# Performance work log

Hardware: AMD Instinct MI355X
Metric: run time of the kernel (lower is better)

The kernel has to match this reference:

```python
import jax, jax.numpy as jnp
import numpy as np

EPS = 1e-10


def setup_inputs() -> dict:
    key = jax.random.key(0)
    k1, k2 = jax.random.split(key)
    B, C, H, W = 8, 16, 256, 256
    x = jax.random.normal(k1, (B, C, H, W), dtype=jnp.float32)
    # grid_sample-style normalized coords in [-1, 1]
    inv_grid = jax.random.uniform(k2, (B, H, W, 2), dtype=jnp.float32, minval=-1.0, maxval=1.0)
    return {"x": x, "inv_grid": inv_grid}


def reference(x, inv_grid):
    B, C, Hin, Win = x.shape
    h, w = Hin, Win  # OH = OW = None -> output size equals input size

    g = (inv_grid + 1.0) * 0.5
    # coord 0 scaled by h, coord 1 by w, shifted by +1 (padding row/col), clamped
    ci = jnp.clip(g[..., 0] * h + 1.0, 0.0, h + 1 - 2 * EPS)
    cj = jnp.clip(g[..., 1] * w + 1.0, 0.0, w + 1 - 2 * EPS)
    i0 = jnp.floor(ci).astype(jnp.int32)  # coords >= 0 so floor == trunc (.long())
    j0 = jnp.floor(cj).astype(jnp.int32)

    # broadcast over channel dim (grid is shared across channels)
    ci_ = ci[:, None]
    cj_ = cj[:, None]
    i0_ = i0[:, None]
    j0_ = j0[:, None]

    bidx = jnp.arange(B)[:, None, None, None]
    cidx = jnp.arange(C)[None, :, None, None]

    A = jnp.zeros((B, C, h + 3, w + 3), dtype=x.dtype)
    for di in range(2):
        wi = jax.nn.relu(1.0 - jnp.abs(ci_ - (i0_ + di).astype(ci_.dtype)))
        for dj in range(2):
            wj = jax.nn.relu(1.0 - jnp.abs(cj_ - (j0_ + dj).astype(cj_.dtype)))
            # bilinear splat scatter-add of x * weight into the 4 corner cells
            A = A.at[bidx, cidx, i0_ + di, j0_ + dj].add(x * (wi * wj))
    return A[..., 1:h + 1, 1:w + 1]
```

## Files before the change

### kernel.cpp

```cpp
#include <hip/hip_runtime.h>
#include <hip/hip_fp16.h>
#include <stdint.h>

#define BB 8
#define CC 16
#define HH 256
#define WW 256
#define HW (HH * WW)
#define NSRC (BB * HW)
#define NBLK (NSRC / 256)
#define MAXSLOT 15
#define CNT_BYTES ((size_t)NSRC * 4)


__global__ __launch_bounds__(256) void pass1_bin(
    const float* __restrict__ inv_grid,
    uint32_t* __restrict__ counts,
    uint2* __restrict__ srcs)
{
    const int idx = blockIdx.x * 256 + threadIdx.x;
    const float2 g2 = ((const float2*)inv_grid)[idx];
    const float ci = fminf(fmaxf(fmaf((g2.x + 1.0f) * 0.5f, (float)HH, 1.0f), 0.0f), 257.0f);
    const float cj = fminf(fmaxf(fmaf((g2.y + 1.0f) * 0.5f, (float)WW, 1.0f), 0.0f), 257.0f);
    const int i0 = (int)floorf(ci);
    const int j0 = (int)floorf(cj);
    const float fi = ci - (float)i0;
    const float fj = cj - (float)j0;
    const int bi = i0 - 1, bj = j0 - 1;
    uint32_t meta = 0xFFFFFFFFu;
    if (((unsigned)bi < HH) & ((unsigned)bj < WW)) {
        const int b = idx >> 16;
        const uint32_t bin = (b << 16) | (bi << 8) | bj;
        const uint32_t slot = atomicAdd(&counts[bin], 1u);
        if (slot < MAXSLOT) meta = (bin << 4) | slot;
    }
    const uint32_t fi16 = (uint32_t)(fi * 65535.0f + 0.5f);
    const uint32_t fj16 = (uint32_t)(fj * 65535.0f + 0.5f);
    uint2 m; m.x = meta; m.y = fi16 | (fj16 << 16);
    srcs[idx] = m;
}

__global__ __launch_bounds__(256) void scanA(
    const uint32_t* __restrict__ counts,
    uint32_t* __restrict__ co,
    uint32_t* __restrict__ cursors)
{
    const int t    = threadIdx.x;
    const int lane = t & 63;
    const int wv   = t >> 6;
    const int blk  = blockIdx.x;
    const int i    = blk * 256 + t;
    const uint32_t v = counts[i];

    uint32_t s = v;
#pragma unroll
    for (int d = 1; d < 64; d <<= 1) {
        const uint32_t u = __shfl_up(s, (unsigned)d, 64);
        if (lane >= d) s += u;
    }

    __shared__ uint32_t wsum[4];
    __shared__ uint32_t gbase_s;
    if (lane == 63) wsum[wv] = s;
    __syncthreads();

    uint32_t base = 0;
#pragma unroll
    for (int w = 0; w < 3; ++w)
        if (w < wv) base += wsum[w];

    if (t == 255) {
        const int b = blk >> 8;
        gbase_s = ((uint32_t)b << 16) + atomicAdd(&cursors[b * 64], base + s);
    }
    __syncthreads();

    const uint32_t excl = base + s - v + gbase_s;
    co[i] = (excl << 4) | min(v, 15u);
}

__global__ __launch_bounds__(256) void fill_records(
    const float* __restrict__ x,
    const uint2* __restrict__ srcs,
    const uint32_t* __restrict__ co,
    uint32_t* __restrict__ ff,
    uint4* __restrict__ pl)
{
    const int idx = blockIdx.x * 256 + threadIdx.x;
    const uint2 m = srcs[idx];
    if (m.x == 0xFFFFFFFFu) return;
    const uint32_t bin  = m.x >> 4;
    const uint32_t slot = m.x & 15u;
    const uint32_t pos  = (co[bin] >> 4) + slot;

    const int b = idx >> 16;
    const int p = idx & 0xFFFF;
    const float* xp = x + (((size_t)b * CC) << 16) + p;

    uint32_t h[8];
#pragma unroll
    for (int q = 0; q < 8; ++q) {
        const float v0 = xp[(size_t)(2 * q)     << 16];
        const float v1 = xp[(size_t)(2 * q + 1) << 16];
        const uint32_t h0 = (uint32_t)__half_as_ushort(__float2half_rn(v0));
        const uint32_t h1 = (uint32_t)__half_as_ushort(__float2half_rn(v1));
        h[q] = h0 | (h1 << 16);
    }
    ff[pos] = m.y;
    uint4 q0; q0.x = h[0]; q0.y = h[1]; q0.z = h[2]; q0.w = h[3];
    uint4 q1; q1.x = h[4]; q1.y = h[5]; q1.z = h[6]; q1.w = h[7];
    pl[(size_t)pos * 2]     = q0;
    pl[(size_t)pos * 2 + 1] = q1;
}

__global__ __launch_bounds__(256) void gather_csr(
    const uint32_t* __restrict__ co,
    const uint32_t* __restrict__ ff,
    const uint4* __restrict__ pl,
    float* __restrict__ out)
{
    const int g   = blockIdx.x;
    const int b   = g & 7;
    const int seq = g >> 3;
    const int r   = ((seq >> 4) << 4) + (threadIdx.x >> 4);
    const int c   = ((seq & 15) << 4) + (threadIdx.x & 15);

    uint32_t hdr[4];
#pragma unroll
    for (int q = 0; q < 4; ++q) {
        const int row = r + (q >> 1) - 1;
        const int col = c + (q & 1) - 1;
        const bool val = (row >= 0) & (col >= 0);
        const uint32_t rr   = val ? (uint32_t)row : 0u;
        const uint32_t ccol = val ? (uint32_t)col : 0u;
        const uint32_t bin = ((uint32_t)b << 16) | (rr << 8) | ccol;
        const uint32_t m = co[bin];
        hdr[q] = val ? m : (m & ~15u);
    }

    float acc[CC];
#pragma unroll
    for (int q = 0; q < CC; ++q) acc[q] = 0.0f;

#pragma unroll
    for (int q = 0; q < 4; ++q) {
        const uint32_t cnt = hdr[q] & 15u;
        const uint32_t off = hdr[q] >> 4;
        for (uint32_t k = 0; k < cnt; ++k) {
            const size_t pos = (size_t)(off + k);
            const uint32_t f2 = ff[pos];
            const uint4 p0 = pl[pos * 2];
            const uint4 p1 = pl[pos * 2 + 1];
            const float fi = (float)(f2 & 0xFFFFu) * (1.0f / 65535.0f);
            const float fj = (float)(f2 >> 16)     * (1.0f / 65535.0f);
            const float wi = (q & 2) ? (1.0f - fi) : fi;
            const float wj = (q & 1) ? (1.0f - fj) : fj;
            const float w = wi * wj;
            const uint32_t hs[8] = {p0.x, p0.y, p0.z, p0.w, p1.x, p1.y, p1.z, p1.w};
#pragma unroll
            for (int qq = 0; qq < 8; ++qq) {
                const float v0 = __half2float(__ushort_as_half((unsigned short)(hs[qq] & 0xFFFFu)));
                const float v1 = __half2float(__ushort_as_half((unsigned short)(hs[qq] >> 16)));
                acc[2 * qq]     += w * v0;
                acc[2 * qq + 1] += w * v1;
            }
        }
    }

    float* op = out + (((size_t)(b * CC)) << 16) + (r << 8) + c;
#pragma unroll
    for (int q = 0; q < CC; ++q)
        op[(size_t)q << 16] = acc[q];
}

__global__ __launch_bounds__(256) void invgrid_scatter_direct(
    const float* __restrict__ x,
    const float* __restrict__ inv_grid,
    float* __restrict__ out)
{
    const int idx = blockIdx.x * 256 + threadIdx.x;
    const int b = idx >> 16;
    const float2 g2 = ((const float2*)inv_grid)[idx];
    const float ci = fminf(fmaxf(fmaf((g2.x + 1.0f) * 0.5f, (float)HH, 1.0f), 0.0f), 257.0f);
    const float cj = fminf(fmaxf(fmaf((g2.y + 1.0f) * 0.5f, (float)WW, 1.0f), 0.0f), 257.0f);
    const int i0 = (int)floorf(ci);
    const int j0 = (int)floorf(cj);
    const float wi0 = fmaxf(0.0f, 1.0f - fabsf(ci - (float)i0));
    const float wi1 = fmaxf(0.0f, 1.0f - fabsf(ci - (float)(i0 + 1)));
    const float wj0 = fmaxf(0.0f, 1.0f - fabsf(cj - (float)j0));
    const float wj1 = fmaxf(0.0f, 1.0f - fabsf(cj - (float)(j0 + 1)));
    const float w00 = wi0 * wj0, w01 = wi0 * wj1;
    const float w10 = wi1 * wj0, w11 = wi1 * wj1;
    const int r0 = i0 - 1, r1 = i0, c0 = j0 - 1, c1 = j0;
    const bool vr0 = (unsigned)r0 < HH, vr1 = (unsigned)r1 < HH;
    const bool vc0 = (unsigned)c0 < WW, vc1 = (unsigned)c1 < WW;
    const int o00 = r0 * WW + c0, o01 = r0 * WW + c1;
    const int o10 = r1 * WW + c0, o11 = r1 * WW + c1;
    const int p = idx & 0xFFFF;
    const float* xp = x + (size_t)b * CC * HW + p;
    float* op = out + (size_t)b * CC * HW;
#pragma unroll
    for (int cch = 0; cch < CC; ++cch) {
        const float xv = xp[(size_t)cch * HW];
        float* ob = op + (size_t)cch * HW;
        if (vr0 & vc0) atomicAdd(ob + o00, xv * w00);
        if (vr0 & vc1) atomicAdd(ob + o01, xv * w01);
        if (vr1 & vc0) atomicAdd(ob + o10, xv * w10);
        if (vr1 & vc1) atomicAdd(ob + o11, xv * w11);
    }
}

extern "C" void kernel_launch(void* const* d_in, const int* in_sizes, int n_in,
                              void* d_out, int out_size, void* d_ws, size_t ws_size,
                              hipStream_t stream) {
    const float* x        = (const float*)d_in[0];
    const float* inv_grid = (const float*)d_in[1];
    float* out            = (float*)d_out;

    const size_t A = 256;
    size_t o_counts  = 0;
    size_t o_cursors = CNT_BYTES;
    size_t o_co      = (CNT_BYTES + 2048 + A - 1) / A * A;
    size_t o_srcs    = o_co   + ((size_t)NSRC * 4 + A - 1) / A * A;
    size_t o_ff      = o_srcs + ((size_t)NSRC * 8 + A - 1) / A * A;
    size_t o_pl      = o_ff   + (CNT_BYTES + A - 1) / A * A;
    size_t need      = o_pl   + (size_t)NSRC * 32;

    if (ws_size >= need) {
        char* w = (char*)d_ws;
        uint32_t* counts  = (uint32_t*)(w + o_counts);
        uint32_t* cursors = (uint32_t*)(w + o_cursors);
        uint32_t* co      = (uint32_t*)(w + o_co);
        uint2*    srcs    = (uint2*)   (w + o_srcs);
        uint32_t* ff      = (uint32_t*)(w + o_ff);
        uint4*    pl      = (uint4*)   (w + o_pl);
        hipMemsetAsync(w, 0, CNT_BYTES + 2048, stream);
        pass1_bin   <<<NBLK, 256, 0, stream>>>(inv_grid, counts, srcs);
        scanA       <<<NBLK, 256, 0, stream>>>(counts, co, cursors);
        fill_records<<<NBLK, 256, 0, stream>>>(x, srcs, co, ff, pl);
        gather_csr  <<<NBLK, 256, 0, stream>>>(co, ff, pl, out);
    } else {
        hipMemsetAsync(d_out, 0, (size_t)out_size * sizeof(float), stream);
        invgrid_scatter_direct<<<NBLK, 256, 0, stream>>>(x, inv_grid, out);
    }
}
```

Before: 151.6 us.

## Fuse the four CSR passes into one persistent kernel with grid barriers

Replaces the memset plus four separate kernel launches with one persistent kernel of 512 blocks. Each block zeroes its share of the counts, then runs binning, scanning, record filling and gathering over four chunks each, with a global atomic-counter barrier between phases. This removes the launch gaps and the large memset, but relies on all 512 blocks being co-resident and adds spin-wait barrier cost. Running fewer blocks, each doing more work, may also reduce latency hiding within each phase.

```diff
diff --git a/kernel.cpp b/kernel.cpp
--- a/kernel.cpp
+++ b/kernel.cpp
@@ -9,16 +9,30 @@
 #define HW (HH * WW)
 #define NSRC (BB * HW)
 #define NBLK (NSRC / 256)
+#define PBLK 512
 #define MAXSLOT 15
 #define CNT_BYTES ((size_t)NSRC * 4)
 
 
-__global__ __launch_bounds__(256) void pass1_bin(
-    const float* __restrict__ inv_grid,
-    uint32_t* __restrict__ counts,
+__device__ __forceinline__ void grid_barrier(uint32_t* bar, uint32_t target)
+{
+    __syncthreads();
+    if (threadIdx.x == 0) {
+        __threadfence();
+        atomicAdd(bar, 1u);
+        while (__hip_atomic_load(bar, __ATOMIC_RELAXED,
+                                 __HIP_MEMORY_SCOPE_AGENT) < target) {
+            __builtin_amdgcn_s_sleep(1);
+        }
+        __threadfence();
+    }
+    __syncthreads();
+}
+
+__device__ __forceinline__ void bin_body(int idx,
+    const float* __restrict__ inv_grid, uint32_t* __restrict__ counts,
     uint2* __restrict__ srcs)
 {
-    const int idx = blockIdx.x * 256 + threadIdx.x;
     const float2 g2 = ((const float2*)inv_grid)[idx];
     const float ci = fminf(fmaxf(fmaf((g2.x + 1.0f) * 0.5f, (float)HH, 1.0f), 0.0f), 257.0f);
     const float cj = fminf(fmaxf(fmaf((g2.y + 1.0f) * 0.5f, (float)WW, 1.0f), 0.0f), 257.0f);
@@ -40,16 +54,13 @@
     srcs[idx] = m;
 }
 
-__global__ __launch_bounds__(256) void scanA(
-    const uint32_t* __restrict__ counts,
-    uint32_t* __restrict__ co,
-    uint32_t* __restrict__ cursors)
-{
-    const int t    = threadIdx.x;
+__device__ __forceinline__ void scan_body(int chunk, int t,
+    const uint32_t* __restrict__ counts, uint32_t* __restrict__ co,
+    uint32_t* __restrict__ cursors, uint32_t* wsum, uint32_t* gbase_s)
+{
     const int lane = t & 63;
     const int wv   = t >> 6;
-    const int blk  = blockIdx.x;
-    const int i    = blk * 256 + t;
+    const int i    = chunk * 256 + t;
     const uint32_t v = counts[i];
 
     uint32_t s = v;
@@ -59,8 +70,6 @@
         if (lane >= d) s += u;
     }
 
-    __shared__ uint32_t wsum[4];
-    __shared__ uint32_t gbase_s;
     if (lane == 63) wsum[wv] = s;
     __syncthreads();
 
@@ -70,60 +79,56 @@
         if (w < wv) base += wsum[w];
 
     if (t == 255) {
-        const int b = blk >> 8;
-        gbase_s = ((uint32_t)b << 16) + atomicAdd(&cursors[b * 64], base + s);
-    }
-    __syncthreads();
-
-    const uint32_t excl = base + s - v + gbase_s;
+        const int b = chunk >> 8;
+        *gbase_s = ((uint32_t)b << 16) + atomicAdd(&cursors[b * 64], base + s);
+    }
+    __syncthreads();
+
+    const uint32_t excl = base + s - v + *gbase_s;
     co[i] = (excl << 4) | min(v, 15u);
-}
-
-__global__ __launch_bounds__(256) void fill_records(
-    const float* __restrict__ x,
-    const uint2* __restrict__ srcs,
-    const uint32_t* __restrict__ co,
-    uint32_t* __restrict__ ff,
+    __syncthreads();
+}
+
+__device__ __forceinline__ void fill_body(int idx,
+    const float* __restrict__ x, const uint2* __restrict__ srcs,
+    const uint32_t* __restrict__ co, uint32_t* __restrict__ ff,
     uint4* __restrict__ pl)
 {
-    const int idx = blockIdx.x * 256 + threadIdx.x;
     const uint2 m = srcs[idx];
-    if (m.x == 0xFFFFFFFFu) return;
-    const uint32_t bin  = m.x >> 4;
-    const uint32_t slot = m.x & 15u;
-    const uint32_t pos  = (co[bin] >> 4) + slot;
-
-    const int b = idx >> 16;
-    const int p = idx & 0xFFFF;
-    const float* xp = x + (((size_t)b * CC) << 16) + p;
-
-    uint32_t h[8];
-#pragma unroll
-    for (int q = 0; q < 8; ++q) {
-        const float v0 = xp[(size_t)(2 * q)     << 16];
-        const float v1 = xp[(size_t)(2 * q + 1) << 16];
-        const uint32_t h0 = (uint32_t)__half_as_ushort(__float2half_rn(v0));
-        const uint32_t h1 = (uint32_t)__half_as_ushort(__float2half_rn(v1));
-        h[q] = h0 | (h1 << 16);
-    }
-    ff[pos] = m.y;
-    uint4 q0; q0.x = h[0]; q0.y = h[1]; q0.z = h[2]; q0.w = h[3];
-    uint4 q1; q1.x = h[4]; q1.y = h[5]; q1.z = h[6]; q1.w = h[7];
-    pl[(size_t)pos * 2]     = q0;
-    pl[(size_t)pos * 2 + 1] = q1;
-}
-
-__global__ __launch_bounds__(256) void gather_csr(
-    const uint32_t* __restrict__ co,
-    const uint32_t* __restrict__ ff,
-    const uint4* __restrict__ pl,
-    float* __restrict__ out)
-{
-    const int g   = blockIdx.x;
+    if (m.x != 0xFFFFFFFFu) {
+        const uint32_t bin  = m.x >> 4;
+        const uint32_t slot = m.x & 15u;
+        const uint32_t pos  = (co[bin] >> 4) + slot;
+
+        const int b = idx >> 16;
+        const int p = idx & 0xFFFF;
+        const float* xp = x + (((size_t)b * CC) << 16) + p;
+
+        uint32_t h[8];
+#pragma unroll
+        for (int q = 0; q < 8; ++q) {
+            const float v0 = xp[(size_t)(2 * q)     << 16];
+            const float v1 = xp[(size_t)(2 * q + 1) << 16];
+            const uint32_t h0 = (uint32_t)__half_as_ushort(__float2half_rn(v0));
+            const uint32_t h1 = (uint32_t)__half_as_ushort(__float2half_rn(v1));
+            h[q] = h0 | (h1 << 16);
+        }
+        ff[pos] = m.y;
+        uint4 q0; q0.x = h[0]; q0.y = h[1]; q0.z = h[2]; q0.w = h[3];
+        uint4 q1; q1.x = h[4]; q1.y = h[5]; q1.z = h[6]; q1.w = h[7];
+        pl[(size_t)pos * 2]     = q0;
+        pl[(size_t)pos * 2 + 1] = q1;
+    }
+}
+
+__device__ __forceinline__ void gather_body(int g, int t,
+    const uint32_t* __restrict__ co, const uint32_t* __restrict__ ff,
+    const uint4* __restrict__ pl, float* __restrict__ out)
+{
     const int b   = g & 7;
     const int seq = g >> 3;
-    const int r   = ((seq >> 4) << 4) + (threadIdx.x >> 4);
-    const int c   = ((seq & 15) << 4) + (threadIdx.x & 15);
+    const int r   = ((seq >> 4) << 4) + (t >> 4);
+    const int c   = ((seq & 15) << 4) + (t & 15);
 
     uint32_t hdr[4];
 #pragma unroll
@@ -171,6 +176,51 @@
 #pragma unroll
     for (int q = 0; q < CC; ++q)
         op[(size_t)q << 16] = acc[q];
+}
+
+__global__ __launch_bounds__(256, 4) void fused_persistent(
+    const float* __restrict__ x,
+    const float* __restrict__ inv_grid,
+    uint32_t* __restrict__ counts,
+    uint32_t* __restrict__ cursors,
+    uint32_t* __restrict__ co,
+    uint2* __restrict__ srcs,
+    uint32_t* __restrict__ ff,
+    uint4* __restrict__ pl,
+    float* __restrict__ out,
+    uint32_t* __restrict__ bar)
+{
+    const int t   = threadIdx.x;
+    const int blk = blockIdx.x;
+
+    {
+        uint4 z; z.x = 0u; z.y = 0u; z.z = 0u; z.w = 0u;
+        ((uint4*)counts)[blk * 256 + t] = z;
+        if (blk == 0) { cursors[t] = 0u; cursors[t + 256] = 0u; }
+    }
+    grid_barrier(bar, PBLK * 1);
+
+#pragma unroll
+    for (int k = 0; k < 4; ++k)
+        bin_body(blk * 1024 + k * 256 + t, inv_grid, counts, srcs);
+    grid_barrier(bar, PBLK * 2);
+
+    {
+        __shared__ uint32_t wsum[4];
+        __shared__ uint32_t gbase_s;
+#pragma unroll
+        for (int k = 0; k < 4; ++k)
+            scan_body(blk * 4 + k, t, counts, co, cursors, wsum, &gbase_s);
+    }
+    grid_barrier(bar, PBLK * 3);
+
+#pragma unroll
+    for (int k = 0; k < 4; ++k)
+        fill_body(blk * 1024 + k * 256 + t, x, srcs, co, ff, pl);
+    grid_barrier(bar, PBLK * 4);
+
+    for (int k = 0; k < 4; ++k)
+        gather_body(blk + PBLK * k, t, co, ff, pl, out);
 }
 
 __global__ __launch_bounds__(256) void invgrid_scatter_direct(
@@ -220,7 +270,8 @@
     const size_t A = 256;
     size_t o_counts  = 0;
     size_t o_cursors = CNT_BYTES;
-    size_t o_co      = (CNT_BYTES + 2048 + A - 1) / A * A;
+    size_t o_bar     = o_cursors + 2048;
+    size_t o_co      = (o_bar + 256 + A - 1) / A * A;
     size_t o_srcs    = o_co   + ((size_t)NSRC * 4 + A - 1) / A * A;
     size_t o_ff      = o_srcs + ((size_t)NSRC * 8 + A - 1) / A * A;
     size_t o_pl      = o_ff   + (CNT_BYTES + A - 1) / A * A;
@@ -230,15 +281,15 @@
         char* w = (char*)d_ws;
         uint32_t* counts  = (uint32_t*)(w + o_counts);
         uint32_t* cursors = (uint32_t*)(w + o_cursors);
+        uint32_t* bar     = (uint32_t*)(w + o_bar);
         uint32_t* co      = (uint32_t*)(w + o_co);
         uint2*    srcs    = (uint2*)   (w + o_srcs);
         uint32_t* ff      = (uint32_t*)(w + o_ff);
         uint4*    pl      = (uint4*)   (w + o_pl);
-        hipMemsetAsync(w, 0, CNT_BYTES + 2048, stream);
-        pass1_bin   <<<NBLK, 256, 0, stream>>>(inv_grid, counts, srcs);
-        scanA       <<<NBLK, 256, 0, stream>>>(counts, co, cursors);
-        fill_records<<<NBLK, 256, 0, stream>>>(x, srcs, co, ff, pl);
-        gather_csr  <<<NBLK, 256, 0, stream>>>(co, ff, pl, out);
+
+        hipMemsetAsync(bar, 0, 256, stream);
+        fused_persistent<<<PBLK, 256, 0, stream>>>(
+            x, inv_grid, counts, cursors, co, srcs, ff, pl, out, bar);
     } else {
         hipMemsetAsync(d_out, 0, (size_t)out_size * sizeof(float), stream);
         invgrid_scatter_direct<<<NBLK, 256, 0, stream>>>(x, inv_grid, out);
```

After: 362.1 us. +138.9%, slower.
